# Kernel optimization log

Measured on AMD Instinct MI355X. Metric: run time of the kernel, lower is better.

Reference implementation:

```python
import jax, jax.numpy as jnp
import numpy as np

EMB = 768
HS = 64
B, T = 4, 4096


def setup_inputs() -> dict:
    key = jax.random.key(0)
    ks = jax.random.split(key, 7)
    s = 1.0 / np.sqrt(EMB)
    return {
        "x": jax.random.normal(ks[0], (B, T, EMB), dtype=jnp.float32),
        "Wk": jax.random.normal(ks[1], (EMB, HS), dtype=jnp.float32) * s,
        "bk": jnp.zeros((HS,), dtype=jnp.float32),
        "Wq": jax.random.normal(ks[2], (EMB, HS), dtype=jnp.float32) * s,
        "bq": jnp.zeros((HS,), dtype=jnp.float32),
        "Wv": jax.random.normal(ks[3], (EMB, HS), dtype=jnp.float32) * s,
        "bv": jnp.zeros((HS,), dtype=jnp.float32),
    }


def reference(x, Wk, bk, Wq, bq, Wv, bv):
    # Linear projections: (B, T, emb) @ (emb, hs) + bias -> (B, T, hs)
    k = x @ Wk + bk
    q = x @ Wq + bq
    v = x @ Wv + bv
    # NOTE: original code computes key @ query^T (k on the left), no 1/sqrt(hs) scaling.
    att = jnp.einsum("bth,bsh->bts", k, q)  # (B, T, T)
    causal = jnp.tril(jnp.ones((T, T), dtype=bool))  # (T, T)
    att = jnp.where(causal, att, -jnp.inf)
    wei = jax.nn.softmax(att, axis=-1)
    return jnp.einsum("bts,bsh->bth", wei, v)  # (B, T, hs)
```

## Files before the change

kernel.cpp:

```cpp
#include <hip/hip_runtime.h>
#include <cmath>

static constexpr int EMB  = 768;
static constexpr int HS   = 64;
static constexpr int NB   = 4;
static constexpr int SEQ  = 4096;
static constexpr int MTOT = NB * SEQ;
static constexpr int SPLITS = 8;

typedef __attribute__((ext_vector_type(8))) short  short8x;
typedef __attribute__((ext_vector_type(4))) float  float4x;
typedef __attribute__((ext_vector_type(4))) unsigned short ushort4x;

__device__ inline unsigned short rne16(float f) {
    unsigned u = __builtin_bit_cast(unsigned, f);
    unsigned r = u + 0x7FFFu + ((u >> 16) & 1u);
    return (unsigned short)(r >> 16);
}
__device__ inline float bf2f(unsigned short h) {
    return __builtin_bit_cast(float, ((unsigned)h) << 16);
}

__global__ __launch_bounds__(256) void convert_w(
    const float* __restrict__ Wk, const float* __restrict__ Wq, const float* __restrict__ Wv,
    unsigned short* __restrict__ wpk)
{
    const int t    = blockIdx.x * 256 + threadIdx.x;
    const int lane = t & 63;
    const int rest = t >> 6;
    const int nng  = rest % 12;
    const int kcp  = rest / 12;
    const int kc   = kcp % 24;
    const int p    = kcp / 24;
    const int which= nng >> 2;
    const int nn   = nng & 3;
    const float* W = (which == 0) ? Wk : (which == 1) ? Wq : Wv;
    const int col  = nn * 16 + (lane & 15);
    const int kr   = kc * 32 + (lane >> 4) * 8;

    unsigned short o[8];
    #pragma unroll
    for (int j = 0; j < 8; ++j) {
        float w = W[(size_t)(kr + j) * HS + col];
        unsigned short h = rne16(w);
        o[j] = (p == 0) ? h : rne16(w - bf2f(h));
    }
    size_t base = ((size_t)((p * 24 + kc) * 12 + nng) * 64 + lane) * 8;
    *(short8x*)&wpk[base] = *(short8x*)o;
}

__global__ __launch_bounds__(256) void proj_kernel(
    const float* __restrict__ x,
    const unsigned short* __restrict__ wpk,
    const float* __restrict__ bk, const float* __restrict__ bq, const float* __restrict__ bv,
    unsigned short* __restrict__ khi, unsigned short* __restrict__ klo,
    unsigned short* __restrict__ qhi, unsigned short* __restrict__ qlo,
    unsigned short* __restrict__ vT)
{
    __shared__ unsigned short xh[2][32 * 72];
    __shared__ unsigned short xl[2][32 * 72];

    const int tid  = threadIdx.x;
    const int lane = tid & 63;
    const int w    = tid >> 6;
    const int l15  = lane & 15;
    const int quad = lane >> 4;
    const int row0 = blockIdx.x * 32;

    float4x acc[3][2] = {};
    float4  pre[2];

    #pragma unroll
    for (int it = 0; it < 2; ++it) {
        const int fi = tid + it * 256;
        const int r  = fi >> 4, c4 = (fi & 15) * 4;
        pre[it] = *(const float4*)&x[(size_t)(row0 + r) * EMB + 0 * 64 + c4];
    }
    #pragma unroll
    for (int it = 0; it < 2; ++it) {
        const int fi = tid + it * 256;
        const int r  = fi >> 4, c4 = (fi & 15) * 4;
        const float4 xv = pre[it];
        const unsigned short h0 = rne16(xv.x), h1 = rne16(xv.y),
                             h2 = rne16(xv.z), h3 = rne16(xv.w);
        ushort4x hv = {h0, h1, h2, h3};
        ushort4x lv = {rne16(xv.x - bf2f(h0)), rne16(xv.y - bf2f(h1)),
                       rne16(xv.z - bf2f(h2)), rne16(xv.w - bf2f(h3))};
        *(ushort4x*)&xh[0][r * 72 + c4] = hv;
        *(ushort4x*)&xl[0][r * 72 + c4] = lv;
    }

    for (int ch = 0; ch < 12; ++ch) {
        if (ch + 1 < 12) {
            #pragma unroll
            for (int it = 0; it < 2; ++it) {
                const int fi = tid + it * 256;
                const int r  = fi >> 4, c4 = (fi & 15) * 4;
                pre[it] = *(const float4*)&x[(size_t)(row0 + r) * EMB + (ch + 1) * 64 + c4];
            }
        }
        __syncthreads();
        const int buf = ch & 1;

        #pragma unroll
        for (int k0i = 0; k0i < 2; ++k0i) {
            const int k0 = k0i * 32;
            const int kc = ch * 2 + k0i;
            short8x ah[2], al[2];
            #pragma unroll
            for (int mi = 0; mi < 2; ++mi) {
                ah[mi] = *(const short8x*)&xh[buf][(mi * 16 + l15) * 72 + k0 + quad * 8];
                al[mi] = *(const short8x*)&xl[buf][(mi * 16 + l15) * 72 + k0 + quad * 8];
            }
            #pragma unroll
            for (int which = 0; which < 3; ++which) {
                const int nng = which * 4 + w;
                const short8x bh = *(const short8x*)&wpk[((size_t)((0 * 24 + kc) * 12 + nng) * 64 + lane) * 8];
                const short8x bl = *(const short8x*)&wpk[((size_t)((1 * 24 + kc) * 12 + nng) * 64 + lane) * 8];
                #pragma unroll
                for (int mi = 0; mi < 2; ++mi) {
                    acc[which][mi] = __builtin_amdgcn_mfma_f32_16x16x32_bf16(ah[mi], bh, acc[which][mi], 0, 0, 0);
                    acc[which][mi] = __builtin_amdgcn_mfma_f32_16x16x32_bf16(ah[mi], bl, acc[which][mi], 0, 0, 0);
                    acc[which][mi] = __builtin_amdgcn_mfma_f32_16x16x32_bf16(al[mi], bh, acc[which][mi], 0, 0, 0);
                }
            }
        }

        if (ch + 1 < 12) {
            const int nbuf = (ch + 1) & 1;
            #pragma unroll
            for (int it = 0; it < 2; ++it) {
                const int fi = tid + it * 256;
                const int r  = fi >> 4, c4 = (fi & 15) * 4;
                const float4 xv = pre[it];
                const unsigned short h0 = rne16(xv.x), h1 = rne16(xv.y),
                                     h2 = rne16(xv.z), h3 = rne16(xv.w);
                ushort4x hv = {h0, h1, h2, h3};
                ushort4x lv = {rne16(xv.x - bf2f(h0)), rne16(xv.y - bf2f(h1)),
                               rne16(xv.z - bf2f(h2)), rne16(xv.w - bf2f(h3))};
                *(ushort4x*)&xh[nbuf][r * 72 + c4] = hv;
                *(ushort4x*)&xl[nbuf][r * 72 + c4] = lv;
            }
        }
    }

    const int col = w * 16 + l15;
    const float bkv = bk[col], bqv = bq[col], bvv = bv[col];
    #pragma unroll
    for (int mi = 0; mi < 2; ++mi) {
        const int rbase = row0 + mi * 16 + quad * 4;
        #pragma unroll
        for (int r = 0; r < 4; ++r) {
            const float kv = acc[0][mi][r] + bkv;
            const unsigned short hk = rne16(kv);
            khi[(size_t)(rbase + r) * 64 + col] = hk;
            klo[(size_t)(rbase + r) * 64 + col] = rne16(kv - bf2f(hk));
            const float qv = acc[1][mi][r] + bqv;
            const unsigned short hq = rne16(qv);
            qhi[(size_t)(rbase + r) * 64 + col] = hq;
            qlo[(size_t)(rbase + r) * 64 + col] = rne16(qv - bf2f(hq));
        }
        const int b = rbase / SEQ;
        const int s = rbase % SEQ;
        ushort4x vv = {rne16(acc[2][mi][0] + bvv), rne16(acc[2][mi][1] + bvv),
                       rne16(acc[2][mi][2] + bvv), rne16(acc[2][mi][3] + bvv)};
        *(ushort4x*)&vT[((size_t)b * 64 + col) * SEQ + s] = vv;
    }
}

__global__ __launch_bounds__(256, 2) void attn_kernel(
    const unsigned short* __restrict__ khi, const unsigned short* __restrict__ klo,
    const unsigned short* __restrict__ qhi, const unsigned short* __restrict__ qlo,
    const unsigned short* __restrict__ vT,
    float* __restrict__ Opart, float* __restrict__ lpart)
{
    __shared__ unsigned short qh_s[2][64 * 72];
    __shared__ unsigned short ql_s[2][64 * 72];
    __shared__ unsigned short vt_s[2][64 * 72];
    __shared__ unsigned short psH[64 * 72];
    __shared__ unsigned short psL[64 * 72];

    const int tid  = threadIdx.x;
    const int lane = tid & 63;
    const int w    = tid >> 6;
    const int l15  = lane & 15;
    const int quad = lane >> 4;

    const int n  = blockIdx.x;
    const int sp = n & (SPLITS - 1);
    const int b  = (n >> 3) & (NB - 1);
    const int p  = n >> 5;
    const int jj[4] = {63 - p, 32 + p, 31 - p, p};
    const size_t rowb = (size_t)b * SEQ;

    float4x oacc[4][4] = {};
    float   l_r[4][4]  = {};

    const int sr = tid >> 3;
    const int c8 = (tid & 7) * 8;

    int cur = 0;
    for (int ci = sp; ci <= jj[0]; ci += SPLITS) {
        const int s0 = ci * 64;
        #pragma unroll
        for (int it = 0; it < 2; ++it) {
            const int r = sr + it * 32;
            *(short8x*)&qh_s[cur][r * 72 + c8] = *(const short8x*)&qhi[(rowb + s0 + r) * 64 + c8];
            *(short8x*)&ql_s[cur][r * 72 + c8] = *(const short8x*)&qlo[(rowb + s0 + r) * 64 + c8];
            *(short8x*)&vt_s[cur][r * 72 + c8] = *(const short8x*)&vT[((size_t)b * 64 + r) * SEQ + s0 + c8];
        }
        __syncthreads();
        const unsigned short* qhc = qh_s[cur];
        const unsigned short* qlc = ql_s[cur];
        const unsigned short* vtc = vt_s[cur];
        cur ^= 1;

        #pragma unroll
        for (int g = 0; g < 2; ++g) {
            const int idxH = g ? 1 : 0;
            const int idxL = g ? 2 : 3;
            const int jH = jj[idxH], jL = jj[idxL];
            const bool aH = (ci <= jH), aL = (ci <= jL);
            if (!aH && !aL) continue;

            short8x ahH[2], alH[2], ahL[2], alL[2];
            #pragma unroll
            for (int k0 = 0; k0 < 2; ++k0) {
                if (aH) {
                    const size_t rH = (rowb + jH * 64 + 16 * w + l15) * 64 + k0 * 32 + quad * 8;
                    ahH[k0] = *(const short8x*)&khi[rH];
                    alH[k0] = *(const short8x*)&klo[rH];
                }
                if (aL) {
                    const size_t rL = (rowb + jL * 64 + 16 * w + l15) * 64 + k0 * 32 + quad * 8;
                    ahL[k0] = *(const short8x*)&khi[rL];
                    alL[k0] = *(const short8x*)&klo[rL];
                }
            }

            float4x sH[4] = {}, sL[4] = {};
            __builtin_amdgcn_s_setprio(1);
            #pragma unroll
            for (int k0 = 0; k0 < 2; ++k0) {
                #pragma unroll
                for (int nn = 0; nn < 4; ++nn) {
                    const short8x bh = *(const short8x*)&qhc[(nn * 16 + l15) * 72 + k0 * 32 + quad * 8];
                    const short8x bl = *(const short8x*)&qlc[(nn * 16 + l15) * 72 + k0 * 32 + quad * 8];
                    if (aH) {
                        sH[nn] = __builtin_amdgcn_mfma_f32_16x16x32_bf16(ahH[k0], bh, sH[nn], 0, 0, 0);
                        sH[nn] = __builtin_amdgcn_mfma_f32_16x16x32_bf16(alH[k0], bh, sH[nn], 0, 0, 0);
                        sH[nn] = __builtin_amdgcn_mfma_f32_16x16x32_bf16(ahH[k0], bl, sH[nn], 0, 0, 0);
                    }
                    if (aL) {
                        sL[nn] = __builtin_amdgcn_mfma_f32_16x16x32_bf16(ahL[k0], bh, sL[nn], 0, 0, 0);
                        sL[nn] = __builtin_amdgcn_mfma_f32_16x16x32_bf16(alL[k0], bh, sL[nn], 0, 0, 0);
                        sL[nn] = __builtin_amdgcn_mfma_f32_16x16x32_bf16(ahL[k0], bl, sL[nn], 0, 0, 0);
                    }
                }
            }
            __builtin_amdgcn_s_setprio(0);

            #pragma unroll
            for (int hl = 0; hl < 2; ++hl) {
                const bool alive = hl ? aL : aH;
                if (!alive) continue;
                const int j   = hl ? jL : jH;
                const int idx = hl ? idxL : idxH;
                float4x* sc   = hl ? sL : sH;
                unsigned short* ps = hl ? psL : psH;
                if (ci == j) {
                    const int trow = j * 64 + 16 * w + quad * 4;
                    #pragma unroll
                    for (int nn = 0; nn < 4; ++nn) {
                        const int colg = s0 + nn * 16 + l15;
                        #pragma unroll
                        for (int r = 0; r < 4; ++r)
                            if (colg > trow + r) sc[nn][r] = -1e30f;
                    }
                }
                #pragma unroll
                for (int nn = 0; nn < 4; ++nn) {
                    #pragma unroll
                    for (int r = 0; r < 4; ++r) {
                        const float e = __expf(fminf(sc[nn][r], 80.0f));
                        const unsigned short h = rne16(e);
                        l_r[idx][r] += bf2f(h);
                        ps[(16 * w + quad * 4 + r) * 72 + nn * 16 + l15] = h;
                    }
                }
            }

            __builtin_amdgcn_s_setprio(1);
            #pragma unroll
            for (int k0 = 0; k0 < 2; ++k0) {
                short8x paH, paL;
                if (aH) paH = *(const short8x*)&psH[(16 * w + l15) * 72 + k0 * 32 + quad * 8];
                if (aL) paL = *(const short8x*)&psL[(16 * w + l15) * 72 + k0 * 32 + quad * 8];
                #pragma unroll
                for (int nn = 0; nn < 4; ++nn) {
                    const short8x vb = *(const short8x*)&vtc[(nn * 16 + l15) * 72 + k0 * 32 + quad * 8];
                    if (aH) oacc[idxH][nn] = __builtin_amdgcn_mfma_f32_16x16x32_bf16(paH, vb, oacc[idxH][nn], 0, 0, 0);
                    if (aL) oacc[idxL][nn] = __builtin_amdgcn_mfma_f32_16x16x32_bf16(paL, vb, oacc[idxL][nn], 0, 0, 0);
                }
            }
            __builtin_amdgcn_s_setprio(0);
        }
    }

    #pragma unroll
    for (int idx = 0; idx < 4; ++idx) {
        const int j = jj[idx];
        if (idx == 3 && sp > p) continue;
        float lv[4];
        #pragma unroll
        for (int r = 0; r < 4; ++r) {
            float l = l_r[idx][r];
            l += __shfl_xor(l, 1);
            l += __shfl_xor(l, 2);
            l += __shfl_xor(l, 4);
            l += __shfl_xor(l, 8);
            lv[r] = l;
        }
        const size_t part = (size_t)(j * NB + b) * SPLITS + sp;
        float* Op = Opart + part * 4096;
        #pragma unroll
        for (int nn = 0; nn < 4; ++nn)
            #pragma unroll
            for (int r = 0; r < 4; ++r)
                Op[(16 * w + quad * 4 + r) * 64 + nn * 16 + l15] = oacc[idx][nn][r];
        if (l15 == 0) {
            #pragma unroll
            for (int r = 0; r < 4; ++r)
                lpart[part * 64 + 16 * w + quad * 4 + r] = lv[r];
        }
    }
}

__global__ __launch_bounds__(256) void combine_kernel(
    const float* __restrict__ Opart, const float* __restrict__ lpart,
    float* __restrict__ out)
{
    const int j   = blockIdx.x;
    const int b   = blockIdx.y;
    const int tid = threadIdx.x;
    const int row = blockIdx.z * 16 + (tid >> 4);
    const int c0  = (tid & 15) * 4;
    const size_t base = (size_t)(j * NB + b) * SPLITS;
    const int spmax = (j >= 16) ? SPLITS : ((j < SPLITS ? j : SPLITS - 1) + 1);

    float4 acc = {0.f, 0.f, 0.f, 0.f};
    float lsum = 0.f;
    for (int sp = 0; sp < spmax; ++sp) {
        lsum += lpart[(base + sp) * 64 + row];
        const float4 v = *(const float4*)&Opart[(base + sp) * 4096 + row * 64 + c0];
        acc.x += v.x; acc.y += v.y; acc.z += v.z; acc.w += v.w;
    }
    const float inv = 1.0f / lsum;
    float4 v;
    v.x = acc.x * inv; v.y = acc.y * inv; v.z = acc.z * inv; v.w = acc.w * inv;
    *(float4*)&out[((size_t)b * SEQ + j * 64 + row) * 64 + c0] = v;
}

extern "C" void kernel_launch(void* const* d_in, const int* in_sizes, int n_in,
                              void* d_out, int out_size, void* d_ws, size_t ws_size,
                              hipStream_t stream)
{
    const float* x  = (const float*)d_in[0];
    const float* Wk = (const float*)d_in[1];
    const float* bk = (const float*)d_in[2];
    const float* Wq = (const float*)d_in[3];
    const float* bq = (const float*)d_in[4];
    const float* Wv = (const float*)d_in[5];
    const float* bv = (const float*)d_in[6];
    float* out = (float*)d_out;

    const size_t NE = (size_t)MTOT * HS;
    unsigned short* khi = (unsigned short*)d_ws;
    unsigned short* klo = khi + NE;
    unsigned short* qhi = klo + NE;
    unsigned short* qlo = qhi + NE;
    unsigned short* vT  = qlo + NE;
    unsigned short* wpk = vT + NE;
    float* Opart = (float*)(wpk + 294912);
    float* lpart = Opart + (size_t)64 * NB * SPLITS * 4096;

    convert_w<<<144, 256, 0, stream>>>(Wk, Wq, Wv, wpk);
    proj_kernel<<<MTOT / 32, 256, 0, stream>>>(x, wpk, bk, bq, bv, khi, klo, qhi, qlo, vT);
    attn_kernel<<<16 * NB * SPLITS, 256, 0, stream>>>(khi, klo, qhi, qlo, vT, Opart, lpart);
    dim3 cgrid(64, NB, 4);
    combine_kernel<<<cgrid, 256, 0, stream>>>(Opart, lpart, out);
}
```

Measured before the change: 155.8 us.

## Fuse weight conversion, projection and attention into one persistent kernel with grid barriers

Merges the weight-packing, QKV projection and split attention kernels into a single 512-block kernel that separates the phases with software grid barriers (atomic counter plus sense flag), reusing one shared-memory buffer. The goal is to remove the launch gaps and tail idle time between the three kernels. It adds a memset launch, spin-wait overhead, and a co-residency requirement: all 512 blocks must be resident at once (2 per CU on 256 CUs) or the barrier deadlocks. The fused kernel also carries a larger shared-memory footprint in the projection phase.

```diff
diff --git a/kernel.cpp b/kernel.cpp
--- a/kernel.cpp
+++ b/kernel.cpp
@@ -7,6 +7,7 @@
 static constexpr int SEQ  = 4096;
 static constexpr int MTOT = NB * SEQ;
 static constexpr int SPLITS = 8;
+static constexpr int GRID  = 512;
 
 typedef __attribute__((ext_vector_type(8))) short  short8x;
 typedef __attribute__((ext_vector_type(4))) float  float4x;
@@ -21,317 +22,329 @@
     return __builtin_bit_cast(float, ((unsigned)h) << 16);
 }
 
-__global__ __launch_bounds__(256) void convert_w(
-    const float* __restrict__ Wk, const float* __restrict__ Wq, const float* __restrict__ Wv,
-    unsigned short* __restrict__ wpk)
-{
-    const int t    = blockIdx.x * 256 + threadIdx.x;
-    const int lane = t & 63;
-    const int rest = t >> 6;
-    const int nng  = rest % 12;
-    const int kcp  = rest / 12;
-    const int kc   = kcp % 24;
-    const int p    = kcp / 24;
-    const int which= nng >> 2;
-    const int nn   = nng & 3;
-    const float* W = (which == 0) ? Wk : (which == 1) ? Wq : Wv;
-    const int col  = nn * 16 + (lane & 15);
-    const int kr   = kc * 32 + (lane >> 4) * 8;
-
-    unsigned short o[8];
-    #pragma unroll
-    for (int j = 0; j < 8; ++j) {
-        float w = W[(size_t)(kr + j) * HS + col];
-        unsigned short h = rne16(w);
-        o[j] = (p == 0) ? h : rne16(w - bf2f(h));
+__device__ inline void grid_barrier(unsigned* cnt, unsigned* sense, unsigned phase) {
+    __syncthreads();
+    if (threadIdx.x == 0) {
+        unsigned arrived = __hip_atomic_fetch_add(cnt, 1u, __ATOMIC_ACQ_REL, __HIP_MEMORY_SCOPE_AGENT);
+        if (arrived == GRID - 1) {
+            __hip_atomic_store(cnt, 0u, __ATOMIC_RELAXED, __HIP_MEMORY_SCOPE_AGENT);
+            __hip_atomic_store(sense, phase, __ATOMIC_RELEASE, __HIP_MEMORY_SCOPE_AGENT);
+        } else {
+            while (__hip_atomic_load(sense, __ATOMIC_ACQUIRE, __HIP_MEMORY_SCOPE_AGENT) < phase)
+                __builtin_amdgcn_s_sleep(2);
+        }
     }
-    size_t base = ((size_t)((p * 24 + kc) * 12 + nng) * 64 + lane) * 8;
-    *(short8x*)&wpk[base] = *(short8x*)o;
-}
-
-__global__ __launch_bounds__(256) void proj_kernel(
+    __syncthreads();
+}
+
+__global__ __launch_bounds__(256, 2) void mega_kernel(
     const float* __restrict__ x,
-    const unsigned short* __restrict__ wpk,
-    const float* __restrict__ bk, const float* __restrict__ bq, const float* __restrict__ bv,
+    const float* __restrict__ Wk, const float* __restrict__ bk,
+    const float* __restrict__ Wq, const float* __restrict__ bq,
+    const float* __restrict__ Wv, const float* __restrict__ bv,
+    unsigned short* __restrict__ wpk,
     unsigned short* __restrict__ khi, unsigned short* __restrict__ klo,
     unsigned short* __restrict__ qhi, unsigned short* __restrict__ qlo,
-    unsigned short* __restrict__ vT)
+    unsigned short* __restrict__ vT,
+    float* __restrict__ Opart, float* __restrict__ lpart,
+    unsigned* __restrict__ bar_cnt, unsigned* __restrict__ bar_sense)
 {
-    __shared__ unsigned short xh[2][32 * 72];
-    __shared__ unsigned short xl[2][32 * 72];
+    __shared__ unsigned short smem[8 * 64 * 72];
 
     const int tid  = threadIdx.x;
     const int lane = tid & 63;
     const int w    = tid >> 6;
     const int l15  = lane & 15;
     const int quad = lane >> 4;
-    const int row0 = blockIdx.x * 32;
-
-    float4x acc[3][2] = {};
-    float4  pre[2];
-
-    #pragma unroll
-    for (int it = 0; it < 2; ++it) {
-        const int fi = tid + it * 256;
-        const int r  = fi >> 4, c4 = (fi & 15) * 4;
-        pre[it] = *(const float4*)&x[(size_t)(row0 + r) * EMB + 0 * 64 + c4];
+
+    {
+        const int gt = blockIdx.x * 256 + tid;
+        if (gt < 36864) {
+            const int cl   = gt & 63;
+            const int rest = gt >> 6;
+            const int nng  = rest % 12;
+            const int kcp  = rest / 12;
+            const int kc   = kcp % 24;
+            const int p    = kcp / 24;
+            const int which= nng >> 2;
+            const int nn   = nng & 3;
+            const float* W = (which == 0) ? Wk : (which == 1) ? Wq : Wv;
+            const int col  = nn * 16 + (cl & 15);
+            const int kr   = kc * 32 + (cl >> 4) * 8;
+            unsigned short o[8];
+            #pragma unroll
+            for (int j = 0; j < 8; ++j) {
+                float wv = W[(size_t)(kr + j) * HS + col];
+                unsigned short h = rne16(wv);
+                o[j] = (p == 0) ? h : rne16(wv - bf2f(h));
+            }
+            size_t base = ((size_t)((p * 24 + kc) * 12 + nng) * 64 + cl) * 8;
+            *(short8x*)&wpk[base] = *(short8x*)o;
+        }
     }
-    #pragma unroll
-    for (int it = 0; it < 2; ++it) {
-        const int fi = tid + it * 256;
-        const int r  = fi >> 4, c4 = (fi & 15) * 4;
-        const float4 xv = pre[it];
-        const unsigned short h0 = rne16(xv.x), h1 = rne16(xv.y),
-                             h2 = rne16(xv.z), h3 = rne16(xv.w);
-        ushort4x hv = {h0, h1, h2, h3};
-        ushort4x lv = {rne16(xv.x - bf2f(h0)), rne16(xv.y - bf2f(h1)),
-                       rne16(xv.z - bf2f(h2)), rne16(xv.w - bf2f(h3))};
-        *(ushort4x*)&xh[0][r * 72 + c4] = hv;
-        *(ushort4x*)&xl[0][r * 72 + c4] = lv;
-    }
-
-    for (int ch = 0; ch < 12; ++ch) {
-        if (ch + 1 < 12) {
-            #pragma unroll
-            for (int it = 0; it < 2; ++it) {
-                const int fi = tid + it * 256;
-                const int r  = fi >> 4, c4 = (fi & 15) * 4;
-                pre[it] = *(const float4*)&x[(size_t)(row0 + r) * EMB + (ch + 1) * 64 + c4];
-            }
-        }
-        __syncthreads();
-        const int buf = ch & 1;
-
-        #pragma unroll
-        for (int k0i = 0; k0i < 2; ++k0i) {
-            const int k0 = k0i * 32;
-            const int kc = ch * 2 + k0i;
-            short8x ah[2], al[2];
-            #pragma unroll
-            for (int mi = 0; mi < 2; ++mi) {
-                ah[mi] = *(const short8x*)&xh[buf][(mi * 16 + l15) * 72 + k0 + quad * 8];
-                al[mi] = *(const short8x*)&xl[buf][(mi * 16 + l15) * 72 + k0 + quad * 8];
-            }
-            #pragma unroll
-            for (int which = 0; which < 3; ++which) {
-                const int nng = which * 4 + w;
-                const short8x bh = *(const short8x*)&wpk[((size_t)((0 * 24 + kc) * 12 + nng) * 64 + lane) * 8];
-                const short8x bl = *(const short8x*)&wpk[((size_t)((1 * 24 + kc) * 12 + nng) * 64 + lane) * 8];
-                #pragma unroll
-                for (int mi = 0; mi < 2; ++mi) {
-                    acc[which][mi] = __builtin_amdgcn_mfma_f32_16x16x32_bf16(ah[mi], bh, acc[which][mi], 0, 0, 0);
-                    acc[which][mi] = __builtin_amdgcn_mfma_f32_16x16x32_bf16(ah[mi], bl, acc[which][mi], 0, 0, 0);
-                    acc[which][mi] = __builtin_amdgcn_mfma_f32_16x16x32_bf16(al[mi], bh, acc[which][mi], 0, 0, 0);
-                }
-            }
-        }
-
-        if (ch + 1 < 12) {
-            const int nbuf = (ch + 1) & 1;
-            #pragma unroll
-            for (int it = 0; it < 2; ++it) {
-                const int fi = tid + it * 256;
-                const int r  = fi >> 4, c4 = (fi & 15) * 4;
-                const float4 xv = pre[it];
-                const unsigned short h0 = rne16(xv.x), h1 = rne16(xv.y),
-                                     h2 = rne16(xv.z), h3 = rne16(xv.w);
-                ushort4x hv = {h0, h1, h2, h3};
-                ushort4x lv = {rne16(xv.x - bf2f(h0)), rne16(xv.y - bf2f(h1)),
-                               rne16(xv.z - bf2f(h2)), rne16(xv.w - bf2f(h3))};
-                *(ushort4x*)&xh[nbuf][r * 72 + c4] = hv;
-                *(ushort4x*)&xl[nbuf][r * 72 + c4] = lv;
-            }
-        }
-    }
-
-    const int col = w * 16 + l15;
-    const float bkv = bk[col], bqv = bq[col], bvv = bv[col];
-    #pragma unroll
-    for (int mi = 0; mi < 2; ++mi) {
-        const int rbase = row0 + mi * 16 + quad * 4;
-        #pragma unroll
-        for (int r = 0; r < 4; ++r) {
-            const float kv = acc[0][mi][r] + bkv;
-            const unsigned short hk = rne16(kv);
-            khi[(size_t)(rbase + r) * 64 + col] = hk;
-            klo[(size_t)(rbase + r) * 64 + col] = rne16(kv - bf2f(hk));
-            const float qv = acc[1][mi][r] + bqv;
-            const unsigned short hq = rne16(qv);
-            qhi[(size_t)(rbase + r) * 64 + col] = hq;
-            qlo[(size_t)(rbase + r) * 64 + col] = rne16(qv - bf2f(hq));
-        }
-        const int b = rbase / SEQ;
-        const int s = rbase % SEQ;
-        ushort4x vv = {rne16(acc[2][mi][0] + bvv), rne16(acc[2][mi][1] + bvv),
-                       rne16(acc[2][mi][2] + bvv), rne16(acc[2][mi][3] + bvv)};
-        *(ushort4x*)&vT[((size_t)b * 64 + col) * SEQ + s] = vv;
-    }
-}
-
-__global__ __launch_bounds__(256, 2) void attn_kernel(
-    const unsigned short* __restrict__ khi, const unsigned short* __restrict__ klo,
-    const unsigned short* __restrict__ qhi, const unsigned short* __restrict__ qlo,
-    const unsigned short* __restrict__ vT,
-    float* __restrict__ Opart, float* __restrict__ lpart)
-{
-    __shared__ unsigned short qh_s[2][64 * 72];
-    __shared__ unsigned short ql_s[2][64 * 72];
-    __shared__ unsigned short vt_s[2][64 * 72];
-    __shared__ unsigned short psH[64 * 72];
-    __shared__ unsigned short psL[64 * 72];
-
-    const int tid  = threadIdx.x;
-    const int lane = tid & 63;
-    const int w    = tid >> 6;
-    const int l15  = lane & 15;
-    const int quad = lane >> 4;
-
-    const int n  = blockIdx.x;
-    const int sp = n & (SPLITS - 1);
-    const int b  = (n >> 3) & (NB - 1);
-    const int p  = n >> 5;
-    const int jj[4] = {63 - p, 32 + p, 31 - p, p};
-    const size_t rowb = (size_t)b * SEQ;
-
-    float4x oacc[4][4] = {};
-    float   l_r[4][4]  = {};
-
-    const int sr = tid >> 3;
-    const int c8 = (tid & 7) * 8;
-
-    int cur = 0;
-    for (int ci = sp; ci <= jj[0]; ci += SPLITS) {
-        const int s0 = ci * 64;
+    grid_barrier(bar_cnt, bar_sense, 1u);
+
+    {
+        auto xh = (unsigned short (*)[32 * 72])(smem);
+        auto xl = (unsigned short (*)[32 * 72])(smem + 2 * 32 * 72);
+        const int row0 = blockIdx.x * 32;
+
+        float4x acc[3][2] = {};
+        float4  pre[2];
+
         #pragma unroll
         for (int it = 0; it < 2; ++it) {
-            const int r = sr + it * 32;
-            *(short8x*)&qh_s[cur][r * 72 + c8] = *(const short8x*)&qhi[(rowb + s0 + r) * 64 + c8];
-            *(short8x*)&ql_s[cur][r * 72 + c8] = *(const short8x*)&qlo[(rowb + s0 + r) * 64 + c8];
-            *(short8x*)&vt_s[cur][r * 72 + c8] = *(const short8x*)&vT[((size_t)b * 64 + r) * SEQ + s0 + c8];
-        }
-        __syncthreads();
-        const unsigned short* qhc = qh_s[cur];
-        const unsigned short* qlc = ql_s[cur];
-        const unsigned short* vtc = vt_s[cur];
-        cur ^= 1;
-
+            const int fi = tid + it * 256;
+            const int r  = fi >> 4, c4 = (fi & 15) * 4;
+            pre[it] = *(const float4*)&x[(size_t)(row0 + r) * EMB + 0 * 64 + c4];
+        }
         #pragma unroll
-        for (int g = 0; g < 2; ++g) {
-            const int idxH = g ? 1 : 0;
-            const int idxL = g ? 2 : 3;
-            const int jH = jj[idxH], jL = jj[idxL];
-            const bool aH = (ci <= jH), aL = (ci <= jL);
-            if (!aH && !aL) continue;
-
-            short8x ahH[2], alH[2], ahL[2], alL[2];
-            #pragma unroll
-            for (int k0 = 0; k0 < 2; ++k0) {
-                if (aH) {
-                    const size_t rH = (rowb + jH * 64 + 16 * w + l15) * 64 + k0 * 32 + quad * 8;
-                    ahH[k0] = *(const short8x*)&khi[rH];
-                    alH[k0] = *(const short8x*)&klo[rH];
-                }
-                if (aL) {
-                    const size_t rL = (rowb + jL * 64 + 16 * w + l15) * 64 + k0 * 32 + quad * 8;
-                    ahL[k0] = *(const short8x*)&khi[rL];
-                    alL[k0] = *(const short8x*)&klo[rL];
-                }
-            }
-
-            float4x sH[4] = {}, sL[4] = {};
-            __builtin_amdgcn_s_setprio(1);
-            #pragma unroll
-            for (int k0 = 0; k0 < 2; ++k0) {
-                #pragma unroll
-                for (int nn = 0; nn < 4; ++nn) {
-                    const short8x bh = *(const short8x*)&qhc[(nn * 16 + l15) * 72 + k0 * 32 + quad * 8];
-                    const short8x bl = *(const short8x*)&qlc[(nn * 16 + l15) * 72 + k0 * 32 + quad * 8];
+        for (int it = 0; it < 2; ++it) {
+            const int fi = tid + it * 256;
+            const int r  = fi >> 4, c4 = (fi & 15) * 4;
+            const float4 xv = pre[it];
+            const unsigned short h0 = rne16(xv.x), h1 = rne16(xv.y),
+                                 h2 = rne16(xv.z), h3 = rne16(xv.w);
+            ushort4x hv = {h0, h1, h2, h3};
+            ushort4x lv = {rne16(xv.x - bf2f(h0)), rne16(xv.y - bf2f(h1)),
+                           rne16(xv.z - bf2f(h2)), rne16(xv.w - bf2f(h3))};
+            *(ushort4x*)&xh[0][r * 72 + c4] = hv;
+            *(ushort4x*)&xl[0][r * 72 + c4] = lv;
+        }
+
+        for (int ch = 0; ch < 12; ++ch) {
+            if (ch + 1 < 12) {
+                #pragma unroll
+                for (int it = 0; it < 2; ++it) {
+                    const int fi = tid + it * 256;
+                    const int r  = fi >> 4, c4 = (fi & 15) * 4;
+                    pre[it] = *(const float4*)&x[(size_t)(row0 + r) * EMB + (ch + 1) * 64 + c4];
+                }
+            }
+            __syncthreads();
+            const int buf = ch & 1;
+
+            #pragma unroll
+            for (int k0i = 0; k0i < 2; ++k0i) {
+                const int k0 = k0i * 32;
+                const int kc = ch * 2 + k0i;
+                short8x ah[2], al[2];
+                #pragma unroll
+                for (int mi = 0; mi < 2; ++mi) {
+                    ah[mi] = *(const short8x*)&xh[buf][(mi * 16 + l15) * 72 + k0 + quad * 8];
+                    al[mi] = *(const short8x*)&xl[buf][(mi * 16 + l15) * 72 + k0 + quad * 8];
+                }
+                #pragma unroll
+                for (int which = 0; which < 3; ++which) {
+                    const int nng = which * 4 + w;
+                    const short8x bh = *(const short8x*)&wpk[((size_t)((0 * 24 + kc) * 12 + nng) * 64 + lane) * 8];
+                    const short8x bl = *(const short8x*)&wpk[((size_t)((1 * 24 + kc) * 12 + nng) * 64 + lane) * 8];
+                    #pragma unroll
+                    for (int mi = 0; mi < 2; ++mi) {
+                        acc[which][mi] = __builtin_amdgcn_mfma_f32_16x16x32_bf16(ah[mi], bh, acc[which][mi], 0, 0, 0);
+                        acc[which][mi] = __builtin_amdgcn_mfma_f32_16x16x32_bf16(ah[mi], bl, acc[which][mi], 0, 0, 0);
+                        acc[which][mi] = __builtin_amdgcn_mfma_f32_16x16x32_bf16(al[mi], bh, acc[which][mi], 0, 0, 0);
+                    }
+                }
+            }
+
+            if (ch + 1 < 12) {
+                const int nbuf = (ch + 1) & 1;
+                #pragma unroll
+                for (int it = 0; it < 2; ++it) {
+                    const int fi = tid + it * 256;
+                    const int r  = fi >> 4, c4 = (fi & 15) * 4;
+                    const float4 xv = pre[it];
+                    const unsigned short h0 = rne16(xv.x), h1 = rne16(xv.y),
+                                         h2 = rne16(xv.z), h3 = rne16(xv.w);
+                    ushort4x hv = {h0, h1, h2, h3};
+                    ushort4x lv = {rne16(xv.x - bf2f(h0)), rne16(xv.y - bf2f(h1)),
+                                   rne16(xv.z - bf2f(h2)), rne16(xv.w - bf2f(h3))};
+                    *(ushort4x*)&xh[nbuf][r * 72 + c4] = hv;
+                    *(ushort4x*)&xl[nbuf][r * 72 + c4] = lv;
+                }
+            }
+        }
+
+        const int col = w * 16 + l15;
+        const float bkv = bk[col], bqv = bq[col], bvv = bv[col];
+        #pragma unroll
+        for (int mi = 0; mi < 2; ++mi) {
+            const int rbase = row0 + mi * 16 + quad * 4;
+            #pragma unroll
+            for (int r = 0; r < 4; ++r) {
+                const float kv = acc[0][mi][r] + bkv;
+                const unsigned short hk = rne16(kv);
+                khi[(size_t)(rbase + r) * 64 + col] = hk;
+                klo[(size_t)(rbase + r) * 64 + col] = rne16(kv - bf2f(hk));
+                const float qv = acc[1][mi][r] + bqv;
+                const unsigned short hq = rne16(qv);
+                qhi[(size_t)(rbase + r) * 64 + col] = hq;
+                qlo[(size_t)(rbase + r) * 64 + col] = rne16(qv - bf2f(hq));
+            }
+            const int b = rbase / SEQ;
+            const int s = rbase % SEQ;
+            ushort4x vv = {rne16(acc[2][mi][0] + bvv), rne16(acc[2][mi][1] + bvv),
+                           rne16(acc[2][mi][2] + bvv), rne16(acc[2][mi][3] + bvv)};
+            *(ushort4x*)&vT[((size_t)b * 64 + col) * SEQ + s] = vv;
+        }
+    }
+    grid_barrier(bar_cnt, bar_sense, 2u);
+
+    {
+        auto qh_s = (unsigned short (*)[64 * 72])(smem);
+        auto ql_s = (unsigned short (*)[64 * 72])(smem + 2 * 64 * 72);
+        auto vt_s = (unsigned short (*)[64 * 72])(smem + 4 * 64 * 72);
+        unsigned short* psH = smem + 6 * 64 * 72;
+        unsigned short* psL = smem + 7 * 64 * 72;
+
+        const int n  = blockIdx.x;
+        const int sp = n & (SPLITS - 1);
+        const int b  = (n >> 3) & (NB - 1);
+        const int p  = n >> 5;
+        const int jj[4] = {63 - p, 32 + p, 31 - p, p};
+        const size_t rowb = (size_t)b * SEQ;
+
+        float4x oacc[4][4] = {};
+        float   l_r[4][4]  = {};
+
+        const int sr = tid >> 3;
+        const int c8 = (tid & 7) * 8;
+
+        int cur = 0;
+        for (int ci = sp; ci <= jj[0]; ci += SPLITS) {
+            const int s0 = ci * 64;
+            #pragma unroll
+            for (int it = 0; it < 2; ++it) {
+                const int r = sr + it * 32;
+                *(short8x*)&qh_s[cur][r * 72 + c8] = *(const short8x*)&qhi[(rowb + s0 + r) * 64 + c8];
+                *(short8x*)&ql_s[cur][r * 72 + c8] = *(const short8x*)&qlo[(rowb + s0 + r) * 64 + c8];
+                *(short8x*)&vt_s[cur][r * 72 + c8] = *(const short8x*)&vT[((size_t)b * 64 + r) * SEQ + s0 + c8];
+            }
+            __syncthreads();
+            const unsigned short* qhc = qh_s[cur];
+            const unsigned short* qlc = ql_s[cur];
+            const unsigned short* vtc = vt_s[cur];
+            cur ^= 1;
+
+            #pragma unroll
+            for (int g = 0; g < 2; ++g) {
+                const int idxH = g ? 1 : 0;
+                const int idxL = g ? 2 : 3;
+                const int jH = jj[idxH], jL = jj[idxL];
+                const bool aH = (ci <= jH), aL = (ci <= jL);
+                if (!aH && !aL) continue;
+
+                short8x ahH[2], alH[2], ahL[2], alL[2];
+                #pragma unroll
+                for (int k0 = 0; k0 < 2; ++k0) {
                     if (aH) {
-                        sH[nn] = __builtin_amdgcn_mfma_f32_16x16x32_bf16(ahH[k0], bh, sH[nn], 0, 0, 0);
-                        sH[nn] = __builtin_amdgcn_mfma_f32_16x16x32_bf16(alH[k0], bh, sH[nn], 0, 0, 0);
-                        sH[nn] = __builtin_amdgcn_mfma_f32_16x16x32_bf16(ahH[k0], bl, sH[nn], 0, 0, 0);
+                        const size_t rH = (rowb + jH * 64 + 16 * w + l15) * 64 + k0 * 32 + quad * 8;
+                        ahH[k0] = *(const short8x*)&khi[rH];
+                        alH[k0] = *(const short8x*)&klo[rH];
                     }
                     if (aL) {
-                        sL[nn] = __builtin_amdgcn_mfma_f32_16x16x32_bf16(ahL[k0], bh, sL[nn], 0, 0, 0);
-                        sL[nn] = __builtin_amdgcn_mfma_f32_16x16x32_bf16(alL[k0], bh, sL[nn], 0, 0, 0);
-                        sL[nn] = __builtin_amdgcn_mfma_f32_16x16x32_bf16(ahL[k0], bl, sL[nn], 0, 0, 0);
-                    }
-                }
-            }
-            __builtin_amdgcn_s_setprio(0);
-
-            #pragma unroll
-            for (int hl = 0; hl < 2; ++hl) {
-                const bool alive = hl ? aL : aH;
-                if (!alive) continue;
-                const int j   = hl ? jL : jH;
-                const int idx = hl ? idxL : idxH;
-                float4x* sc   = hl ? sL : sH;
-                unsigned short* ps = hl ? psL : psH;
-                if (ci == j) {
-                    const int trow = j * 64 + 16 * w + quad * 4;
+                        const size_t rL = (rowb + jL * 64 + 16 * w + l15) * 64 + k0 * 32 + quad * 8;
+                        ahL[k0] = *(const short8x*)&khi[rL];
+                        alL[k0] = *(const short8x*)&klo[rL];
+                    }
+                }
+
+                float4x sH[4] = {}, sL[4] = {};
+                __builtin_amdgcn_s_setprio(1);
+                #pragma unroll
+                for (int k0 = 0; k0 < 2; ++k0) {
                     #pragma unroll
                     for (int nn = 0; nn < 4; ++nn) {
-                        const int colg = s0 + nn * 16 + l15;
+                        const short8x bh = *(const short8x*)&qhc[(nn * 16 + l15) * 72 + k0 * 32 + quad * 8];
+                        const short8x bl = *(const short8x*)&qlc[(nn * 16 + l15) * 72 + k0 * 32 + quad * 8];
+                        if (aH) {
+                            sH[nn] = __builtin_amdgcn_mfma_f32_16x16x32_bf16(ahH[k0], bh, sH[nn], 0, 0, 0);
+                            sH[nn] = __builtin_amdgcn_mfma_f32_16x16x32_bf16(alH[k0], bh, sH[nn], 0, 0, 0);
+                            sH[nn] = __builtin_amdgcn_mfma_f32_16x16x32_bf16(ahH[k0], bl, sH[nn], 0, 0, 0);
+                        }
+                        if (aL) {
+                            sL[nn] = __builtin_amdgcn_mfma_f32_16x16x32_bf16(ahL[k0], bh, sL[nn], 0, 0, 0);
+                            sL[nn] = __builtin_amdgcn_mfma_f32_16x16x32_bf16(alL[k0], bh, sL[nn], 0, 0, 0);
+                            sL[nn] = __builtin_amdgcn_mfma_f32_16x16x32_bf16(ahL[k0], bl, sL[nn], 0, 0, 0);
+                        }
+                    }
+                }
+                __builtin_amdgcn_s_setprio(0);
+
+                #pragma unroll
+                for (int hl = 0; hl < 2; ++hl) {
+                    const bool alive = hl ? aL : aH;
+                    if (!alive) continue;
+                    const int j   = hl ? jL : jH;
+                    const int idx = hl ? idxL : idxH;
+                    float4x* sc   = hl ? sL : sH;
+                    unsigned short* ps = hl ? psL : psH;
+                    if (ci == j) {
+                        const int trow = j * 64 + 16 * w + quad * 4;
                         #pragma unroll
-                        for (int r = 0; r < 4; ++r)
-                            if (colg > trow + r) sc[nn][r] = -1e30f;
-                    }
-                }
-                #pragma unroll
-                for (int nn = 0; nn < 4; ++nn) {
+                        for (int nn = 0; nn < 4; ++nn) {
+                            const int colg = s0 + nn * 16 + l15;
+                            #pragma unroll
+                            for (int r = 0; r < 4; ++r)
+                                if (colg > trow + r) sc[nn][r] = -1e30f;
+                        }
+                    }
                     #pragma unroll
-                    for (int r = 0; r < 4; ++r) {
-                        const float e = __expf(fminf(sc[nn][r], 80.0f));
-                        const unsigned short h = rne16(e);
-                        l_r[idx][r] += bf2f(h);
-                        ps[(16 * w + quad * 4 + r) * 72 + nn * 16 + l15] = h;
-                    }
-                }
-            }
-
-            __builtin_amdgcn_s_setprio(1);
-            #pragma unroll
-            for (int k0 = 0; k0 < 2; ++k0) {
-                short8x paH, paL;
-                if (aH) paH = *(const short8x*)&psH[(16 * w + l15) * 72 + k0 * 32 + quad * 8];
-                if (aL) paL = *(const short8x*)&psL[(16 * w + l15) * 72 + k0 * 32 + quad * 8];
-                #pragma unroll
-                for (int nn = 0; nn < 4; ++nn) {
-                    const short8x vb = *(const short8x*)&vtc[(nn * 16 + l15) * 72 + k0 * 32 + quad * 8];
-                    if (aH) oacc[idxH][nn] = __builtin_amdgcn_mfma_f32_16x16x32_bf16(paH, vb, oacc[idxH][nn], 0, 0, 0);
-                    if (aL) oacc[idxL][nn] = __builtin_amdgcn_mfma_f32_16x16x32_bf16(paL, vb, oacc[idxL][nn], 0, 0, 0);
-                }
-            }
-            __builtin_amdgcn_s_setprio(0);
-        }
-    }
-
-    #pragma unroll
-    for (int idx = 0; idx < 4; ++idx) {
-        const int j = jj[idx];
-        if (idx == 3 && sp > p) continue;
-        float lv[4];
+                    for (int nn = 0; nn < 4; ++nn) {
+                        #pragma unroll
+                        for (int r = 0; r < 4; ++r) {
+                            const float e = __expf(fminf(sc[nn][r], 80.0f));
+                            const unsigned short h = rne16(e);
+                            l_r[idx][r] += bf2f(h);
+                            ps[(16 * w + quad * 4 + r) * 72 + nn * 16 + l15] = h;
+                        }
+                    }
+                }
+
+                __builtin_amdgcn_s_setprio(1);
+                #pragma unroll
+                for (int k0 = 0; k0 < 2; ++k0) {
+                    short8x paH, paL;
+                    if (aH) paH = *(const short8x*)&psH[(16 * w + l15) * 72 + k0 * 32 + quad * 8];
+                    if (aL) paL = *(const short8x*)&psL[(16 * w + l15) * 72 + k0 * 32 + quad * 8];
+                    #pragma unroll
+                    for (int nn = 0; nn < 4; ++nn) {
+                        const short8x vb = *(const short8x*)&vtc[(nn * 16 + l15) * 72 + k0 * 32 + quad * 8];
+                        if (aH) oacc[idxH][nn] = __builtin_amdgcn_mfma_f32_16x16x32_bf16(paH, vb, oacc[idxH][nn], 0, 0, 0);
+                        if (aL) oacc[idxL][nn] = __builtin_amdgcn_mfma_f32_16x16x32_bf16(paL, vb, oacc[idxL][nn], 0, 0, 0);
+                    }
+                }
+                __builtin_amdgcn_s_setprio(0);
+            }
+        }
+
         #pragma unroll
-        for (int r = 0; r < 4; ++r) {
-            float l = l_r[idx][r];
-            l += __shfl_xor(l, 1);
-            l += __shfl_xor(l, 2);
-            l += __shfl_xor(l, 4);
-            l += __shfl_xor(l, 8);
-            lv[r] = l;
-        }
-        const size_t part = (size_t)(j * NB + b) * SPLITS + sp;
-        float* Op = Opart + part * 4096;
-        #pragma unroll
-        for (int nn = 0; nn < 4; ++nn)
-            #pragma unroll
-            for (int r = 0; r < 4; ++r)
-                Op[(16 * w + quad * 4 + r) * 64 + nn * 16 + l15] = oacc[idx][nn][r];
-        if (l15 == 0) {
-            #pragma unroll
-            for (int r = 0; r < 4; ++r)
-                lpart[part * 64 + 16 * w + quad * 4 + r] = lv[r];
+        for (int idx = 0; idx < 4; ++idx) {
+            const int j = jj[idx];
+            if (idx == 3 && sp > p) continue;
+            float lv[4];
+            #pragma unroll
+            for (int r = 0; r < 4; ++r) {
+                float l = l_r[idx][r];
+                l += __shfl_xor(l, 1);
+                l += __shfl_xor(l, 2);
+                l += __shfl_xor(l, 4);
+                l += __shfl_xor(l, 8);
+                lv[r] = l;
+            }
+            const size_t part = (size_t)(j * NB + b) * SPLITS + sp;
+            float* Op = Opart + part * 4096;
+            #pragma unroll
+            for (int nn = 0; nn < 4; ++nn)
+                #pragma unroll
+                for (int r = 0; r < 4; ++r)
+                    Op[(16 * w + quad * 4 + r) * 64 + nn * 16 + l15] = oacc[idx][nn][r];
+            if (l15 == 0) {
+                #pragma unroll
+                for (int r = 0; r < 4; ++r)
+                    lpart[part * 64 + 16 * w + quad * 4 + r] = lv[r];
+            }
         }
     }
 }
@@ -383,10 +396,12 @@
     unsigned short* wpk = vT + NE;
     float* Opart = (float*)(wpk + 294912);
     float* lpart = Opart + (size_t)64 * NB * SPLITS * 4096;
-
-    convert_w<<<144, 256, 0, stream>>>(Wk, Wq, Wv, wpk);
-    proj_kernel<<<MTOT / 32, 256, 0, stream>>>(x, wpk, bk, bq, bv, khi, klo, qhi, qlo, vT);
-    attn_kernel<<<16 * NB * SPLITS, 256, 0, stream>>>(khi, klo, qhi, qlo, vT, Opart, lpart);
+    unsigned* bar = (unsigned*)(lpart + (size_t)64 * NB * SPLITS * 64);
+
+    hipMemsetAsync(bar, 0, 2 * sizeof(unsigned), stream);
+    mega_kernel<<<GRID, 256, 0, stream>>>(x, Wk, bk, Wq, bq, Wv, bv,
+                                          wpk, khi, klo, qhi, qlo, vT,
+                                          Opart, lpart, bar, bar + 1);
     dim3 cgrid(64, NB, 4);
     combine_kernel<<<cgrid, 256, 0, stream>>>(Opart, lpart, out);
 }
```

Result: slower. 292.2 us (+87.6%).
